# Performance work log

Measured on AMD Instinct MI355X. Metric: run time of the kernel, lower is better.

The kernel has to match this reference:

```python
import jax, jax.numpy as jnp
import numpy as np

TOPK = 2
RENORMALIZE = True

T, H, I, E = 2048, 2048, 5632, 8  # tokens, hidden, intermediate, experts


def setup_inputs() -> dict:
    key = jax.random.key(0)
    k1, k2, k3, k4 = jax.random.split(key, 4)
    x = jax.random.normal(k1, (T, H), dtype=jnp.float32)
    gating_output = jax.random.normal(k2, (T, E), dtype=jnp.float32)
    # gate_up_proj: concat of gate [E,I,H] and up [E,I,H] along dim 1 -> [E,2I,H]
    w1 = jax.random.normal(k3, (E, 2 * I, H), dtype=jnp.float32) * 0.02
    # down_proj: [E, H, I]
    w2 = jax.random.normal(k4, (E, H, I), dtype=jnp.float32) * 0.02
    return {"x": x, "gating_output": gating_output, "w1": w1, "w2": w2}


def _route(gating_output):
    # standard (non-grouped) top-k softmax routing, renormalized
    probs = jax.nn.softmax(gating_output, axis=-1)            # [T, E]
    topk_w, topk_idx = jax.lax.top_k(probs, TOPK)             # [T, K]
    if RENORMALIZE:
        topk_w = topk_w / jnp.sum(topk_w, axis=-1, keepdims=True)
    t = gating_output.shape[0]
    route = jnp.zeros((t, gating_output.shape[1]), dtype=topk_w.dtype)
    route = route.at[jnp.arange(t)[:, None], topk_idx].set(topk_w)  # [T, E]
    return route


def reference(x, gating_output, w1, w2):
    route = _route(gating_output)                             # [T, E]
    inter = w2.shape[-1]
    out = jnp.zeros_like(x)
    # loop over small fixed expert count; each iter is dense GEMM work
    for e in range(w1.shape[0]):
        gu = x @ w1[e].T                                      # [T, 2I]
        h = jax.nn.silu(gu[:, :inter]) * gu[:, inter:]        # SwiGLU  [T, I]
        out = out + (h @ w2[e].T) * route[:, e:e + 1]         # [T, H]
    return out
```

## Files before the change

kernel.cpp:

```cpp
#include <hip/hip_runtime.h>
#include <hip/hip_bf16.h>


#define TT 2048
#define HH 2048
#define II 5632
#define NE 8

using f32x4  = __attribute__((ext_vector_type(4))) float;
using bf16x8 = __attribute__((ext_vector_type(8))) short;

__device__ __forceinline__ uint32_t bfbits(float f) {
    __hip_bfloat16 h = __float2bfloat16(f);
    unsigned short u;
    __builtin_memcpy(&u, &h, 2);
    return (uint32_t)u;
}
__device__ __forceinline__ uint32_t pk2(float a, float b) {
    return bfbits(a) | (bfbits(b) << 16);
}
__device__ __forceinline__ uint4 pk8(const float4& a, const float4& b) {
    uint4 r;
    r.x = pk2(a.x, a.y); r.y = pk2(a.z, a.w);
    r.z = pk2(b.x, b.y); r.w = pk2(b.z, b.w);
    return r;
}
__device__ __forceinline__ void gl16(const void* g, void* l) {
    __builtin_amdgcn_global_load_lds(
        (const __attribute__((address_space(1))) unsigned int*)g,
        (__attribute__((address_space(3))) unsigned int*)l, 16, 0, 0);
}

__global__ void cvt_x(const float* __restrict__ x, __hip_bfloat16* __restrict__ xb) {
    const int i = (blockIdx.x * 256 + threadIdx.x) * 8;
    float4 a = *(const float4*)(x + i);
    float4 b = *(const float4*)(x + i + 4);
    *(uint4*)(xb + i) = pk8(a, b);
}

__global__ void route_topk(const float* __restrict__ gating,
                           int* __restrict__ tk_idx, float* __restrict__ tk_w) {
    int t = blockIdx.x * 256 + threadIdx.x;
    if (t >= TT) return;
    float g[NE];
#pragma unroll
    for (int e = 0; e < NE; e++) g[e] = gating[t * NE + e];
    int i0 = 0; float b0 = g[0];
#pragma unroll
    for (int e = 1; e < NE; e++) if (g[e] > b0) { b0 = g[e]; i0 = e; }
    int i1 = (i0 == 0) ? 1 : 0; float b1 = g[i1];
#pragma unroll
    for (int e = 0; e < NE; e++) if (e != i0 && g[e] > b1) { b1 = g[e]; i1 = e; }
    float ex = expf(b1 - b0);
    float w0 = 1.f / (1.f + ex);
    float w1 = ex / (1.f + ex);
    tk_idx[2 * t] = i0; tk_idx[2 * t + 1] = i1;
    tk_w[2 * t] = w0;  tk_w[2 * t + 1] = w1;
}

__global__ void build_lists(const int* __restrict__ tk_idx, const float* __restrict__ tk_w,
                            int* __restrict__ list_tok, float* __restrict__ list_w,
                            int* __restrict__ counts) {
    const int e = blockIdx.x;
    const int tid = threadIdx.x;
    int flag[8]; float wt[8];
    int cnt = 0;
#pragma unroll
    for (int j = 0; j < 8; j++) {
        int t = tid * 8 + j;
        int f = -1;
        if (tk_idx[2 * t] == e) f = 0;
        else if (tk_idx[2 * t + 1] == e) f = 1;
        flag[j] = f;
        wt[j] = (f >= 0) ? tk_w[2 * t + f] : 0.f;
        cnt += (f >= 0) ? 1 : 0;
    }
    __shared__ int s[256];
    s[tid] = cnt;
    __syncthreads();
    for (int d = 1; d < 256; d <<= 1) {
        int v = (tid >= d) ? s[tid - d] : 0;
        __syncthreads();
        s[tid] += v;
        __syncthreads();
    }
    int pos = s[tid] - cnt;
#pragma unroll
    for (int j = 0; j < 8; j++) {
        if (flag[j] >= 0) {
            list_tok[e * TT + pos] = tid * 8 + j;
            list_w[e * TT + pos] = wt[j];
            pos++;
        }
    }
    if (tid == 255) counts[e] = s[255];
}

__global__ __launch_bounds__(512, 4) void gemm1_swiglu(
    const __hip_bfloat16* __restrict__ xb, const float* __restrict__ w1,
    const int* __restrict__ list_tok, const int* __restrict__ counts,
    __hip_bfloat16* __restrict__ hbuf) {
    const int e = blockIdx.y >> 3;
    const int mt = blockIdx.y & 7;
    const int cnt = counts[e];
    const int row0 = mt * 256;
    if (row0 >= cnt) return;
    int off = 0;
#pragma unroll
    for (int i = 0; i < NE; i++) if (i < e) off += counts[i];
    const int valid = min(256, cnt - row0);
    const int n0 = blockIdx.x * 64;
    const int tid = threadIdx.x;
    const int w = tid >> 6, l = tid & 63;

    __shared__ uint4 As[2 * 1024];
    __shared__ uint4 Bs[2][512];

    const char *aSrc0, *aSrc1;
    {
        int r0 = w * 16 + (l >> 2);
        int r1 = r0 + 128;
        int t0 = list_tok[e * TT + row0 + min(r0, valid - 1)];
        int t1 = list_tok[e * TT + row0 + min(r1, valid - 1)];
        int s0 = (l & 3) ^ ((r0 >> 1) & 3);
        int s1 = (l & 3) ^ ((r1 >> 1) & 3);
        aSrc0 = (const char*)(xb + (size_t)t0 * HH + s0 * 8);
        aSrc1 = (const char*)(xb + (size_t)t1 * HH + s1 * 8);
    }
    auto STAGEA = [&](int kt, int b) {
        char* ab = (char*)As + b * 16384 + w * 1024;
        gl16(aSrc0 + (size_t)kt * 64, ab);
        gl16(aSrc1 + (size_t)kt * 64, ab + 8192);
    };

    const int br = tid >> 2, bu2 = tid & 3;
    const float* bSrc;
    {
        const float* base = w1 + (size_t)e * (2 * II) * HH;
        int r = (br < 64) ? (n0 + br) : (II + n0 + (br - 64));
        bSrc = base + (size_t)r * HH + bu2 * 8;
    }
    const int bwi = br * 4 + (bu2 ^ ((br >> 1) & 3));

    float4 rBa, rBb;
    auto LOADB = [&](int kt) {
        const int k = kt * 32;
        rBa = *(const float4*)(bSrc + k); rBb = *(const float4*)(bSrc + k + 4);
    };
    auto STOREB = [&](int b) { Bs[b][bwi] = pk8(rBa, rBb); };

    const int wm = w >> 1, wn = w & 1;
    const int l15 = l & 15, ks = l >> 4;
    int aidx[4], bgidx[2], buidx[2];
#pragma unroll
    for (int m = 0; m < 4; m++) { int r = wm * 64 + m * 16 + l15; aidx[m] = r * 4 + (ks ^ ((r >> 1) & 3)); }
#pragma unroll
    for (int n = 0; n < 2; n++) {
        int cg = wn * 32 + n * 16 + l15;
        int cu = cg + 64;
        bgidx[n] = cg * 4 + (ks ^ ((cg >> 1) & 3));
        buidx[n] = cu * 4 + (ks ^ ((cu >> 1) & 3));
    }

    f32x4 accg[4][2], accu[4][2];
#pragma unroll
    for (int m = 0; m < 4; m++)
#pragma unroll
        for (int n = 0; n < 2; n++) { accg[m][n] = 0; accu[m][n] = 0; }

    STAGEA(0, 0); LOADB(0); STOREB(0);
    __syncthreads();
    const int KT = HH / 32;
#pragma unroll 2
    for (int kt = 0; kt < KT; ++kt) {
        const int cur = kt & 1;
        if (kt + 1 < KT) {
            STAGEA(kt + 1, cur ^ 1);
            LOADB(kt + 1);
        }
        bf16x8 gf[2], uf[2];
#pragma unroll
        for (int n = 0; n < 2; n++) {
            uint4 t = Bs[cur][bgidx[n]]; gf[n] = __builtin_bit_cast(bf16x8, t);
            uint4 t2 = Bs[cur][buidx[n]]; uf[n] = __builtin_bit_cast(bf16x8, t2);
        }
        const uint4* Ab = As + cur * 1024;
#pragma unroll
        for (int m = 0; m < 4; m++) {
            uint4 t = Ab[aidx[m]];
            bf16x8 af = __builtin_bit_cast(bf16x8, t);
#pragma unroll
            for (int n = 0; n < 2; n++) {
                accg[m][n] = __builtin_amdgcn_mfma_f32_16x16x32_bf16(af, gf[n], accg[m][n], 0, 0, 0);
                accu[m][n] = __builtin_amdgcn_mfma_f32_16x16x32_bf16(af, uf[n], accu[m][n], 0, 0, 0);
            }
        }
        if (kt + 1 < KT) STOREB(cur ^ 1);
        __syncthreads();
    }

#pragma unroll
    for (int m = 0; m < 4; m++) {
#pragma unroll
        for (int r = 0; r < 4; r++) {
            const int lr = wm * 64 + m * 16 + ks * 4 + r;
            if (lr < valid) {
                __hip_bfloat16* hrow = hbuf + (size_t)(off + row0 + lr) * II;
#pragma unroll
                for (int n = 0; n < 2; n++) {
                    const int col = n0 + wn * 32 + n * 16 + l15;
                    float g = accg[m][n][r], u = accu[m][n][r];
                    float h = g / (1.f + __expf(-g)) * u;
                    hrow[col] = __float2bfloat16(h);
                }
            }
        }
    }
}

__global__ __launch_bounds__(512, 4) void gemm2_scatter(
    const __hip_bfloat16* __restrict__ hbuf, const float* __restrict__ w2,
    const int* __restrict__ list_tok, const float* __restrict__ list_w,
    const int* __restrict__ counts, float* __restrict__ out) {
    const int e = blockIdx.y >> 3;
    const int mt = blockIdx.y & 7;
    const int cnt = counts[e];
    const int row0 = mt * 256;
    if (row0 >= cnt) return;
    int off = 0;
#pragma unroll
    for (int i = 0; i < NE; i++) if (i < e) off += counts[i];
    const int valid = min(256, cnt - row0);
    const int n0 = blockIdx.x * 128;
    const int tid = threadIdx.x;
    const int w = tid >> 6, l = tid & 63;

    __shared__ uint4 As[2 * 1024];
    __shared__ uint4 Bs[2][512];

    const char *aSrc0, *aSrc1;
    {
        int r0 = w * 16 + (l >> 2);
        int r1 = r0 + 128;
        int s0 = (l & 3) ^ ((r0 >> 1) & 3);
        int s1 = (l & 3) ^ ((r1 >> 1) & 3);
        aSrc0 = (const char*)(hbuf + (size_t)(off + row0 + min(r0, valid - 1)) * II + s0 * 8);
        aSrc1 = (const char*)(hbuf + (size_t)(off + row0 + min(r1, valid - 1)) * II + s1 * 8);
    }
    auto STAGEA = [&](int kt, int b) {
        char* ab = (char*)As + b * 16384 + w * 1024;
        gl16(aSrc0 + (size_t)kt * 64, ab);
        gl16(aSrc1 + (size_t)kt * 64, ab + 8192);
    };

    const int br = tid >> 2, bu2 = tid & 3;
    const float* bSrc = w2 + (size_t)e * HH * II + (size_t)(n0 + br) * II + bu2 * 8;
    const int bwi = br * 4 + (bu2 ^ ((br >> 1) & 3));

    float4 rBa, rBb;
    auto LOADB = [&](int kt) {
        const int k = kt * 32;
        rBa = *(const float4*)(bSrc + k); rBb = *(const float4*)(bSrc + k + 4);
    };
    auto STOREB = [&](int b) { Bs[b][bwi] = pk8(rBa, rBb); };

    const int wm = w >> 2, wn = w & 3;
    const int l15 = l & 15, ks = l >> 4;
    int aidx[8], bidx[2];
#pragma unroll
    for (int m = 0; m < 8; m++) { int r = wm * 128 + m * 16 + l15; aidx[m] = r * 4 + (ks ^ ((r >> 1) & 3)); }
#pragma unroll
    for (int n = 0; n < 2; n++) { int c = wn * 32 + n * 16 + l15; bidx[n] = c * 4 + (ks ^ ((c >> 1) & 3)); }

    f32x4 acc[8][2];
#pragma unroll
    for (int m = 0; m < 8; m++)
#pragma unroll
        for (int n = 0; n < 2; n++) acc[m][n] = 0;

    STAGEA(0, 0); LOADB(0); STOREB(0);
    __syncthreads();
    const int KT = II / 32;
#pragma unroll 2
    for (int kt = 0; kt < KT; ++kt) {
        const int cur = kt & 1;
        if (kt + 1 < KT) {
            STAGEA(kt + 1, cur ^ 1);
            LOADB(kt + 1);
        }
        bf16x8 bf[2];
#pragma unroll
        for (int n = 0; n < 2; n++) { uint4 t = Bs[cur][bidx[n]]; bf[n] = __builtin_bit_cast(bf16x8, t); }
        const uint4* Ab = As + cur * 1024;
#pragma unroll
        for (int m = 0; m < 8; m++) {
            uint4 t = Ab[aidx[m]];
            bf16x8 af = __builtin_bit_cast(bf16x8, t);
#pragma unroll
            for (int n = 0; n < 2; n++)
                acc[m][n] = __builtin_amdgcn_mfma_f32_16x16x32_bf16(af, bf[n], acc[m][n], 0, 0, 0);
        }
        if (kt + 1 < KT) STOREB(cur ^ 1);
        __syncthreads();
    }

#pragma unroll
    for (int m = 0; m < 8; m++) {
#pragma unroll
        for (int r = 0; r < 4; r++) {
            const int lr = wm * 128 + m * 16 + ks * 4 + r;
            if (lr < valid) {
                const int tok = list_tok[e * TT + row0 + lr];
                const float wt = list_w[e * TT + row0 + lr];
                float* orow = out + (size_t)tok * HH;
#pragma unroll
                for (int n = 0; n < 2; n++) {
                    const int col = n0 + wn * 32 + n * 16 + l15;
                    atomicAdd(orow + col, acc[m][n][r] * wt);
                }
            }
        }
    }
}

extern "C" void kernel_launch(void* const* d_in, const int* in_sizes, int n_in,
                              void* d_out, int out_size, void* d_ws, size_t ws_size,
                              hipStream_t stream) {
    const float* x      = (const float*)d_in[0];
    const float* gating = (const float*)d_in[1];
    const float* w1     = (const float*)d_in[2];
    const float* w2     = (const float*)d_in[3];
    float* out = (float*)d_out;
    char* ws = (char*)d_ws;

    int*   list_tok = (int*)(ws + 0);
    float* list_w   = (float*)(ws + (64 << 10));
    int*   counts   = (int*)(ws + (128 << 10));
    int*   tk_idx   = (int*)(ws + (132 << 10));
    float* tk_w     = (float*)(ws + (148 << 10));
    __hip_bfloat16* hbuf = (__hip_bfloat16*)(ws + (1 << 20));

    __hip_bfloat16* xb = (__hip_bfloat16*)d_out;

    route_topk<<<TT / 256, 256, 0, stream>>>(gating, tk_idx, tk_w);
    build_lists<<<NE, 256, 0, stream>>>(tk_idx, tk_w, list_tok, list_w, counts);
    cvt_x<<<TT * HH / (256 * 8), 256, 0, stream>>>(x, xb);
    gemm1_swiglu<<<dim3(II / 64, NE * 8), 512, 0, stream>>>(xb, w1, list_tok, counts, hbuf);
    (void)hipMemsetAsync(d_out, 0, (size_t)TT * HH * sizeof(float), stream);
    gemm2_scatter<<<dim3(HH / 128, NE * 8), 512, 0, stream>>>(hbuf, w2, list_tok, list_w, counts, out);
}
```

Before: 689.8 us.

## Double block tile width to 1024-thread blocks in both expert GEMMs

Both GEMM kernels move to 1024-thread blocks with twice the output-column tile (gemm1: 128 gate+128 up columns, gemm2: 256 columns), so each staged A tile of token rows is reused across more columns. In gemm2 the warp layout becomes 4x4 MFMA fragments per wave instead of 8x2. This halves the number of times the gathered activation rows are streamed from memory per output. In exchange it adds register and LDS pressure and lowers the block count per GPU, which can reduce occupancy and latency hiding.

```diff
diff --git a/kernel.cpp b/kernel.cpp
--- a/kernel.cpp
+++ b/kernel.cpp
@@ -96,7 +96,7 @@
     if (tid == 255) counts[e] = s[255];
 }
 
-__global__ __launch_bounds__(512, 4) void gemm1_swiglu(
+__global__ __launch_bounds__(1024, 4) void gemm1_swiglu(
     const __hip_bfloat16* __restrict__ xb, const float* __restrict__ w1,
     const int* __restrict__ list_tok, const int* __restrict__ counts,
     __hip_bfloat16* __restrict__ hbuf) {
@@ -109,35 +109,29 @@
 #pragma unroll
     for (int i = 0; i < NE; i++) if (i < e) off += counts[i];
     const int valid = min(256, cnt - row0);
-    const int n0 = blockIdx.x * 64;
+    const int n0 = blockIdx.x * 128;
     const int tid = threadIdx.x;
     const int w = tid >> 6, l = tid & 63;
 
     __shared__ uint4 As[2 * 1024];
-    __shared__ uint4 Bs[2][512];
-
-    const char *aSrc0, *aSrc1;
+    __shared__ uint4 Bs[2 * 1024];
+
+    const char* aSrc;
     {
-        int r0 = w * 16 + (l >> 2);
-        int r1 = r0 + 128;
-        int t0 = list_tok[e * TT + row0 + min(r0, valid - 1)];
-        int t1 = list_tok[e * TT + row0 + min(r1, valid - 1)];
-        int s0 = (l & 3) ^ ((r0 >> 1) & 3);
-        int s1 = (l & 3) ^ ((r1 >> 1) & 3);
-        aSrc0 = (const char*)(xb + (size_t)t0 * HH + s0 * 8);
-        aSrc1 = (const char*)(xb + (size_t)t1 * HH + s1 * 8);
+        int r = w * 16 + (l >> 2);
+        int t0 = list_tok[e * TT + row0 + min(r, valid - 1)];
+        int s0 = (l & 3) ^ ((r >> 1) & 3);
+        aSrc = (const char*)(xb + (size_t)t0 * HH + s0 * 8);
     }
     auto STAGEA = [&](int kt, int b) {
-        char* ab = (char*)As + b * 16384 + w * 1024;
-        gl16(aSrc0 + (size_t)kt * 64, ab);
-        gl16(aSrc1 + (size_t)kt * 64, ab + 8192);
+        gl16(aSrc + (size_t)kt * 64, (char*)As + b * 16384 + w * 1024);
     };
 
     const int br = tid >> 2, bu2 = tid & 3;
     const float* bSrc;
     {
         const float* base = w1 + (size_t)e * (2 * II) * HH;
-        int r = (br < 64) ? (n0 + br) : (II + n0 + (br - 64));
+        int r = (br < 128) ? (n0 + br) : (II + n0 + (br - 128));
         bSrc = base + (size_t)r * HH + bu2 * 8;
     }
     const int bwi = br * 4 + (bu2 ^ ((br >> 1) & 3));
@@ -147,9 +141,9 @@
         const int k = kt * 32;
         rBa = *(const float4*)(bSrc + k); rBb = *(const float4*)(bSrc + k + 4);
     };
-    auto STOREB = [&](int b) { Bs[b][bwi] = pk8(rBa, rBb); };
-
-    const int wm = w >> 1, wn = w & 1;
+    auto STOREB = [&](int b) { Bs[b * 1024 + bwi] = pk8(rBa, rBb); };
+
+    const int wm = w >> 2, wn = w & 3;
     const int l15 = l & 15, ks = l >> 4;
     int aidx[4], bgidx[2], buidx[2];
 #pragma unroll
@@ -157,7 +151,7 @@
 #pragma unroll
     for (int n = 0; n < 2; n++) {
         int cg = wn * 32 + n * 16 + l15;
-        int cu = cg + 64;
+        int cu = cg + 128;
         bgidx[n] = cg * 4 + (ks ^ ((cg >> 1) & 3));
         buidx[n] = cu * 4 + (ks ^ ((cu >> 1) & 3));
     }
@@ -181,8 +175,8 @@
         bf16x8 gf[2], uf[2];
 #pragma unroll
         for (int n = 0; n < 2; n++) {
-            uint4 t = Bs[cur][bgidx[n]]; gf[n] = __builtin_bit_cast(bf16x8, t);
-            uint4 t2 = Bs[cur][buidx[n]]; uf[n] = __builtin_bit_cast(bf16x8, t2);
+            uint4 t = Bs[cur * 1024 + bgidx[n]]; gf[n] = __builtin_bit_cast(bf16x8, t);
+            uint4 t2 = Bs[cur * 1024 + buidx[n]]; uf[n] = __builtin_bit_cast(bf16x8, t2);
         }
         const uint4* Ab = As + cur * 1024;
 #pragma unroll
@@ -218,7 +212,7 @@
     }
 }
 
-__global__ __launch_bounds__(512, 4) void gemm2_scatter(
+__global__ __launch_bounds__(1024, 4) void gemm2_scatter(
     const __hip_bfloat16* __restrict__ hbuf, const float* __restrict__ w2,
     const int* __restrict__ list_tok, const float* __restrict__ list_w,
     const int* __restrict__ counts, float* __restrict__ out) {
@@ -231,26 +225,21 @@
 #pragma unroll
     for (int i = 0; i < NE; i++) if (i < e) off += counts[i];
     const int valid = min(256, cnt - row0);
-    const int n0 = blockIdx.x * 128;
+    const int n0 = blockIdx.x * 256;
     const int tid = threadIdx.x;
     const int w = tid >> 6, l = tid & 63;
 
     __shared__ uint4 As[2 * 1024];
-    __shared__ uint4 Bs[2][512];
-
-    const char *aSrc0, *aSrc1;
+    __shared__ uint4 Bs[2 * 1024];
+
+    const char* aSrc;
     {
-        int r0 = w * 16 + (l >> 2);
-        int r1 = r0 + 128;
-        int s0 = (l & 3) ^ ((r0 >> 1) & 3);
-        int s1 = (l & 3) ^ ((r1 >> 1) & 3);
-        aSrc0 = (const char*)(hbuf + (size_t)(off + row0 + min(r0, valid - 1)) * II + s0 * 8);
-        aSrc1 = (const char*)(hbuf + (size_t)(off + row0 + min(r1, valid - 1)) * II + s1 * 8);
+        int r = w * 16 + (l >> 2);
+        int s0 = (l & 3) ^ ((r >> 1) & 3);
+        aSrc = (const char*)(hbuf + (size_t)(off + row0 + min(r, valid - 1)) * II + s0 * 8);
     }
     auto STAGEA = [&](int kt, int b) {
-        char* ab = (char*)As + b * 16384 + w * 1024;
-        gl16(aSrc0 + (size_t)kt * 64, ab);
-        gl16(aSrc1 + (size_t)kt * 64, ab + 8192);
+        gl16(aSrc + (size_t)kt * 64, (char*)As + b * 16384 + w * 1024);
     };
 
     const int br = tid >> 2, bu2 = tid & 3;
@@ -262,21 +251,21 @@
         const int k = kt * 32;
         rBa = *(const float4*)(bSrc + k); rBb = *(const float4*)(bSrc + k + 4);
     };
-    auto STOREB = [&](int b) { Bs[b][bwi] = pk8(rBa, rBb); };
+    auto STOREB = [&](int b) { Bs[b * 1024 + bwi] = pk8(rBa, rBb); };
 
     const int wm = w >> 2, wn = w & 3;
     const int l15 = l & 15, ks = l >> 4;
-    int aidx[8], bidx[2];
-#pragma unroll
-    for (int m = 0; m < 8; m++) { int r = wm * 128 + m * 16 + l15; aidx[m] = r * 4 + (ks ^ ((r >> 1) & 3)); }
-#pragma unroll
-    for (int n = 0; n < 2; n++) { int c = wn * 32 + n * 16 + l15; bidx[n] = c * 4 + (ks ^ ((c >> 1) & 3)); }
-
-    f32x4 acc[8][2];
-#pragma unroll
-    for (int m = 0; m < 8; m++)
-#pragma unroll
-        for (int n = 0; n < 2; n++) acc[m][n] = 0;
+    int aidx[4], bidx[4];
+#pragma unroll
+    for (int m = 0; m < 4; m++) { int r = wm * 64 + m * 16 + l15; aidx[m] = r * 4 + (ks ^ ((r >> 1) & 3)); }
+#pragma unroll
+    for (int n = 0; n < 4; n++) { int c = wn * 64 + n * 16 + l15; bidx[n] = c * 4 + (ks ^ ((c >> 1) & 3)); }
+
+    f32x4 acc[4][4];
+#pragma unroll
+    for (int m = 0; m < 4; m++)
+#pragma unroll
+        for (int n = 0; n < 4; n++) acc[m][n] = 0;
 
     STAGEA(0, 0); LOADB(0); STOREB(0);
     __syncthreads();
@@ -288,16 +277,16 @@
             STAGEA(kt + 1, cur ^ 1);
             LOADB(kt + 1);
         }
-        bf16x8 bf[2];
-#pragma unroll
-        for (int n = 0; n < 2; n++) { uint4 t = Bs[cur][bidx[n]]; bf[n] = __builtin_bit_cast(bf16x8, t); }
+        bf16x8 bf[4];
+#pragma unroll
+        for (int n = 0; n < 4; n++) { uint4 t = Bs[cur * 1024 + bidx[n]]; bf[n] = __builtin_bit_cast(bf16x8, t); }
         const uint4* Ab = As + cur * 1024;
 #pragma unroll
-        for (int m = 0; m < 8; m++) {
+        for (int m = 0; m < 4; m++) {
             uint4 t = Ab[aidx[m]];
             bf16x8 af = __builtin_bit_cast(bf16x8, t);
 #pragma unroll
-            for (int n = 0; n < 2; n++)
+            for (int n = 0; n < 4; n++)
                 acc[m][n] = __builtin_amdgcn_mfma_f32_16x16x32_bf16(af, bf[n], acc[m][n], 0, 0, 0);
         }
         if (kt + 1 < KT) STOREB(cur ^ 1);
@@ -305,17 +294,17 @@
     }
 
 #pragma unroll
-    for (int m = 0; m < 8; m++) {
+    for (int m = 0; m < 4; m++) {
 #pragma unroll
         for (int r = 0; r < 4; r++) {
-            const int lr = wm * 128 + m * 16 + ks * 4 + r;
+            const int lr = wm * 64 + m * 16 + ks * 4 + r;
             if (lr < valid) {
                 const int tok = list_tok[e * TT + row0 + lr];
                 const float wt = list_w[e * TT + row0 + lr];
                 float* orow = out + (size_t)tok * HH;
 #pragma unroll
-                for (int n = 0; n < 2; n++) {
-                    const int col = n0 + wn * 32 + n * 16 + l15;
+                for (int n = 0; n < 4; n++) {
+                    const int col = n0 + wn * 64 + n * 16 + l15;
                     atomicAdd(orow + col, acc[m][n][r] * wt);
                 }
             }
@@ -345,7 +334,7 @@
     route_topk<<<TT / 256, 256, 0, stream>>>(gating, tk_idx, tk_w);
     build_lists<<<NE, 256, 0, stream>>>(tk_idx, tk_w, list_tok, list_w, counts);
     cvt_x<<<TT * HH / (256 * 8), 256, 0, stream>>>(x, xb);
-    gemm1_swiglu<<<dim3(II / 64, NE * 8), 512, 0, stream>>>(xb, w1, list_tok, counts, hbuf);
+    gemm1_swiglu<<<dim3(II / 128, NE * 8), 1024, 0, stream>>>(xb, w1, list_tok, counts, hbuf);
     (void)hipMemsetAsync(d_out, 0, (size_t)TT * HH * sizeof(float), stream);
-    gemm2_scatter<<<dim3(HH / 128, NE * 8), 512, 0, stream>>>(hbuf, w2, list_tok, list_w, counts, out);
-}
+    gemm2_scatter<<<dim3(HH / 256, NE * 8), 1024, 0, stream>>>(hbuf, w2, list_tok, list_w, counts, out);
+}
```

After: 734.8 us. +6.5%, slower.

## Replace atomic scatter in down-projection with row buffer plus gather combine

Applied to the files above, without the earlier changes.

The down-projection GEMM now writes unweighted per-row results into a dense workspace buffer instead of atomically adding weighted values into the output. A new combine kernel looks up each token's two rows through an inverse index, weights them and writes the output once with vector stores. The output memset goes away. The aim is to remove fp32 atomic contention and the scattered atomic traffic. In exchange, an extra 4096x2048 fp32 buffer is written and read back, and one more kernel is launched.

```diff
diff --git a/kernel.cpp b/kernel.cpp
--- a/kernel.cpp
+++ b/kernel.cpp
@@ -59,11 +59,11 @@
 }
 
 __global__ void build_lists(const int* __restrict__ tk_idx, const float* __restrict__ tk_w,
-                            int* __restrict__ list_tok, float* __restrict__ list_w,
+                            int* __restrict__ list_tok, int* __restrict__ inv,
                             int* __restrict__ counts) {
     const int e = blockIdx.x;
     const int tid = threadIdx.x;
-    int flag[8]; float wt[8];
+    int flag[8];
     int cnt = 0;
 #pragma unroll
     for (int j = 0; j < 8; j++) {
@@ -72,7 +72,6 @@
         if (tk_idx[2 * t] == e) f = 0;
         else if (tk_idx[2 * t + 1] == e) f = 1;
         flag[j] = f;
-        wt[j] = (f >= 0) ? tk_w[2 * t + f] : 0.f;
         cnt += (f >= 0) ? 1 : 0;
     }
     __shared__ int s[256];
@@ -88,8 +87,9 @@
 #pragma unroll
     for (int j = 0; j < 8; j++) {
         if (flag[j] >= 0) {
-            list_tok[e * TT + pos] = tid * 8 + j;
-            list_w[e * TT + pos] = wt[j];
+            int t = tid * 8 + j;
+            list_tok[e * TT + pos] = t;
+            inv[2 * t + flag[j]] = e * TT + pos;
             pos++;
         }
     }
@@ -218,10 +218,9 @@
     }
 }
 
-__global__ __launch_bounds__(512, 4) void gemm2_scatter(
+__global__ __launch_bounds__(512, 4) void gemm2_rows(
     const __hip_bfloat16* __restrict__ hbuf, const float* __restrict__ w2,
-    const int* __restrict__ list_tok, const float* __restrict__ list_w,
-    const int* __restrict__ counts, float* __restrict__ out) {
+    const int* __restrict__ counts, float* __restrict__ gbuf) {
     const int e = blockIdx.y >> 3;
     const int mt = blockIdx.y & 7;
     const int cnt = counts[e];
@@ -310,17 +309,45 @@
         for (int r = 0; r < 4; r++) {
             const int lr = wm * 128 + m * 16 + ks * 4 + r;
             if (lr < valid) {
-                const int tok = list_tok[e * TT + row0 + lr];
-                const float wt = list_w[e * TT + row0 + lr];
-                float* orow = out + (size_t)tok * HH;
+                float* orow = gbuf + (size_t)(off + row0 + lr) * HH;
 #pragma unroll
                 for (int n = 0; n < 2; n++) {
                     const int col = n0 + wn * 32 + n * 16 + l15;
-                    atomicAdd(orow + col, acc[m][n][r] * wt);
+                    orow[col] = acc[m][n][r];
                 }
             }
         }
     }
+}
+
+__global__ void combine(const float* __restrict__ gbuf, const int* __restrict__ inv,
+                        const float* __restrict__ tk_w, const int* __restrict__ counts,
+                        float* __restrict__ out) {
+    const int idx = blockIdx.x * 256 + threadIdx.x;
+    const int t = idx >> 8;
+    const int c = (idx & 255) * 8;
+    int offs[NE];
+    {
+        int s = 0;
+#pragma unroll
+        for (int e = 0; e < NE; e++) { offs[e] = s; s += counts[e]; }
+    }
+    const int i0 = inv[2 * t], i1 = inv[2 * t + 1];
+    const float w0 = tk_w[2 * t], w1 = tk_w[2 * t + 1];
+    const float* g0 = gbuf + (size_t)(offs[i0 >> 11] + (i0 & 2047)) * HH + c;
+    const float* g1 = gbuf + (size_t)(offs[i1 >> 11] + (i1 & 2047)) * HH + c;
+    float4 a0 = *(const float4*)(g0);
+    float4 a1 = *(const float4*)(g0 + 4);
+    float4 b0 = *(const float4*)(g1);
+    float4 b1 = *(const float4*)(g1 + 4);
+    float4 o0, o1;
+    o0.x = w0 * a0.x + w1 * b0.x; o0.y = w0 * a0.y + w1 * b0.y;
+    o0.z = w0 * a0.z + w1 * b0.z; o0.w = w0 * a0.w + w1 * b0.w;
+    o1.x = w0 * a1.x + w1 * b1.x; o1.y = w0 * a1.y + w1 * b1.y;
+    o1.z = w0 * a1.z + w1 * b1.z; o1.w = w0 * a1.w + w1 * b1.w;
+    float* op = out + (size_t)t * HH + c;
+    *(float4*)(op) = o0;
+    *(float4*)(op + 4) = o1;
 }
 
 extern "C" void kernel_launch(void* const* d_in, const int* in_sizes, int n_in,
@@ -334,18 +361,19 @@
     char* ws = (char*)d_ws;
 
     int*   list_tok = (int*)(ws + 0);
-    float* list_w   = (float*)(ws + (64 << 10));
-    int*   counts   = (int*)(ws + (128 << 10));
-    int*   tk_idx   = (int*)(ws + (132 << 10));
-    float* tk_w     = (float*)(ws + (148 << 10));
+    int*   inv      = (int*)(ws + (64 << 10));
+    int*   counts   = (int*)(ws + (96 << 10));
+    int*   tk_idx   = (int*)(ws + (100 << 10));
+    float* tk_w     = (float*)(ws + (116 << 10));
     __hip_bfloat16* hbuf = (__hip_bfloat16*)(ws + (1 << 20));
+    float* gbuf = (float*)(ws + (size_t)(64 << 20));
 
     __hip_bfloat16* xb = (__hip_bfloat16*)d_out;
 
     route_topk<<<TT / 256, 256, 0, stream>>>(gating, tk_idx, tk_w);
-    build_lists<<<NE, 256, 0, stream>>>(tk_idx, tk_w, list_tok, list_w, counts);
+    build_lists<<<NE, 256, 0, stream>>>(tk_idx, tk_w, list_tok, inv, counts);
     cvt_x<<<TT * HH / (256 * 8), 256, 0, stream>>>(x, xb);
     gemm1_swiglu<<<dim3(II / 64, NE * 8), 512, 0, stream>>>(xb, w1, list_tok, counts, hbuf);
-    (void)hipMemsetAsync(d_out, 0, (size_t)TT * HH * sizeof(float), stream);
-    gemm2_scatter<<<dim3(HH / 128, NE * 8), 512, 0, stream>>>(hbuf, w2, list_tok, list_w, counts, out);
-}
+    gemm2_rows<<<dim3(HH / 128, NE * 8), 512, 0, stream>>>(hbuf, w2, counts, gbuf);
+    combine<<<TT * HH / (256 * 8), 256, 0, stream>>>(gbuf, inv, tk_w, counts, out);
+}
```

New measurement: 675.2 us. -2.1%, faster.
